# Performance work log

Hardware: AMD Instinct MI355X
Metric: run time of the kernel (lower is better)

Reference implementation:

```python
import jax, jax.numpy as jnp
import numpy as np

N, C_IN, H, W = 256, 256, 28, 28
D = 64        # prototype channel dim (prototype_shape[1])
P = 200       # num prototypes
NCLS = 10


def setup_inputs() -> dict:
    key = jax.random.key(0)
    ks = jax.random.split(key, 6)
    x = jax.random.normal(ks[0], (N, C_IN, H, W), dtype=jnp.float32)
    W1 = jax.random.normal(ks[1], (D, C_IN), dtype=jnp.float32) * 0.05
    b1 = jnp.zeros((D,), dtype=jnp.float32)
    W2 = jax.random.normal(ks[2], (D, D), dtype=jnp.float32) * 0.05
    b2 = jnp.zeros((D,), dtype=jnp.float32)
    prototypes = jax.random.uniform(ks[3], (P, D), dtype=jnp.float32)
    last_W = jax.random.normal(ks[4], (NCLS, P), dtype=jnp.float32) * 0.05
    last_b = jnp.zeros((NCLS,), dtype=jnp.float32)
    return {"x": x, "W1": W1, "b1": b1, "W2": W2, "b2": b2,
            "prototypes": prototypes, "last_W": last_W, "last_b": last_b}


def reference(x, W1, b1, W2, b2, prototypes, last_W, last_b):
    # add_on_layers: 1x1 conv -> relu -> 1x1 conv -> sigmoid (pointwise GEMMs)
    h = jax.nn.relu(jnp.einsum('nchw,oc->nohw', x, W1) + b1[None, :, None, None])
    f = jax.nn.sigmoid(jnp.einsum('nchw,oc->nohw', h, W2) + b2[None, :, None, None])
    # L2 convolution with 1x1 prototypes:
    # conv(x^2, ones) == channel sum of f^2, broadcast over P prototypes
    x2_patch_sum = jnp.sum(f * f, axis=1, keepdims=True)          # (N,1,H,W)
    xp = jnp.einsum('nchw,pc->nphw', f, prototypes)               # (N,P,H,W)
    p2 = jnp.sum(prototypes * prototypes, axis=1)[None, :, None, None]  # (1,P,1,1)
    distances = jax.nn.relu(x2_patch_sum - 2.0 * xp + p2)         # (N,P,H,W)
    # global min-pool over spatial dims (== -maxpool(-d) with full kernel)
    min_distances = jnp.min(distances, axis=(2, 3))               # (N,P)
    # paf == 'linear': similarity = -distance
    prototype_activations = -min_distances
    logits = prototype_activations @ last_W.T + last_b            # (N,NCLS)
    return (logits, min_distances)
```

## Files before the change

kernel.cpp:

```cpp
#include <hip/hip_runtime.h>
#include <hip/hip_bf16.h>

#define NIMG 256
#define CIN  256
#define PIX  784
#define DD   64
#define NP   200
#define NPP  208
#define NCLS 10

#define XS 264
#define HS 72

typedef __attribute__((ext_vector_type(8))) short bf16x8;
typedef __attribute__((ext_vector_type(4))) float f32x4;
typedef __attribute__((ext_vector_type(4))) unsigned int u32x4;

__device__ __forceinline__ unsigned short f2bf(float f) {
    union { float f; unsigned int u; } v; v.f = f;
    unsigned int r = v.u + 0x7fffu + ((v.u >> 16) & 1u);
    return (unsigned short)(r >> 16);
}

__device__ __forceinline__ unsigned int pk2(float a, float b) {
    __hip_bfloat162 p = __float22bfloat162_rn(make_float2(a, b));
    return *(unsigned int*)&p;
}

#define MFMA(a, b, c) __builtin_amdgcn_mfma_f32_16x16x32_bf16((a), (b), (c), 0, 0, 0)

__global__ __launch_bounds__(512, 2)
void proto_fused_kernel(const float* __restrict__ x,
                        const float* __restrict__ W1, const float* __restrict__ b1,
                        const float* __restrict__ W2, const float* __restrict__ b2,
                        const float* __restrict__ proto,
                        const float* __restrict__ lastW, const float* __restrict__ lastb,
                        float* __restrict__ out)
{
    __shared__ __align__(16) unsigned short xlds[64 * XS];
    __shared__ __align__(16) unsigned short w1lds[64 * XS];
    __shared__ __align__(16) unsigned short w2lds[64 * HS];
    __shared__ __align__(16) unsigned short protolds[NPP * HS];
    __shared__ __align__(16) unsigned short htile[64 * HS];
    __shared__ __align__(16) unsigned short ftile[64 * HS];
    __shared__ float p2lds[NPP];
    __shared__ float s2lds[2][64];
    __shared__ float b1lds[DD], b2lds[DD];
    __shared__ unsigned int bmin[NPP];

    const int n    = blockIdx.x;
    const int t    = threadIdx.x;
    const int lane = t & 63;
    const int q    = lane >> 4;
    const int l15  = lane & 15;
    const int wave = t >> 6;
    const int s    = wave & 3;
    const int dh   = wave >> 2;
    const int dt0  = dh * 2, dt1 = dh * 2 + 1;

    for (int i = 0; i < 32; ++i) {
        int idx = t + i * 512;
        w1lds[(idx >> 8) * XS + (idx & 255)] = f2bf(W1[idx]);
    }
    for (int i = 0; i < 8; ++i) {
        int idx = t + i * 512;
        w2lds[(idx >> 6) * HS + (idx & 63)] = f2bf(W2[idx]);
    }
    for (int i = 0; i < 25; ++i) {
        int idx = t + i * 512;
        protolds[(idx >> 6) * HS + (idx & 63)] = f2bf(proto[idx]);
    }
    {
        int p = NP + (t >> 6), d = t & 63;
        protolds[p * HS + d] = 0;
    }
    if (t < DD) { b1lds[t] = b1[t]; b2lds[t] = b2[t]; }
    if (t < NPP) {
        float acc = 0.f;
        if (t < NP) {
            for (int d = 0; d < DD; ++d) { float v = proto[t * DD + d]; acc += v * v; }
        }
        p2lds[t] = acc;
        bmin[t] = 0x7f800000u;
    }

    const int p4  = (t & 15) * 4;
    const int cb8 = (t >> 4) * 8;
    const float* xn = x + (size_t)n * CIN * PIX;

    float4 pf[8];
    auto load_tile = [&](int px0) {
        #pragma unroll
        for (int j = 0; j < 8; ++j) {
            const float* src = xn + (size_t)(cb8 + j) * PIX + px0 + p4;
            float4 v;
            if (px0 + p4 + 3 < PIX) {
                v = *(const float4*)src;
            } else {
                v.x = (px0 + p4 + 0 < PIX) ? src[0] : 0.f;
                v.y = (px0 + p4 + 1 < PIX) ? src[1] : 0.f;
                v.z = (px0 + p4 + 2 < PIX) ? src[2] : 0.f;
                v.w = (px0 + p4 + 3 < PIX) ? src[3] : 0.f;
            }
            pf[j] = v;
        }
    };
    auto store_tile = [&]() {
        #pragma unroll
        for (int r = 0; r < 4; ++r) {
            u32x4 uv;
            uv.x = pk2(((const float*)&pf[0])[r], ((const float*)&pf[1])[r]);
            uv.y = pk2(((const float*)&pf[2])[r], ((const float*)&pf[3])[r]);
            uv.z = pk2(((const float*)&pf[4])[r], ((const float*)&pf[5])[r]);
            uv.w = pk2(((const float*)&pf[6])[r], ((const float*)&pf[7])[r]);
            *(u32x4*)&xlds[(p4 + r) * XS + cb8] = uv;
        }
    };

    load_tile(0);
    store_tile();
    load_tile(64);
    __syncthreads();

    bf16x8 w1f0[8], w1f1[8];
    #pragma unroll
    for (int kk = 0; kk < 8; ++kk) {
        w1f0[kk] = *(const bf16x8*)&w1lds[(dt0 * 16 + l15) * XS + kk * 32 + q * 8];
        w1f1[kk] = *(const bf16x8*)&w1lds[(dt1 * 16 + l15) * XS + kk * 32 + q * 8];
    }
    bf16x8 w2f0[2], w2f1[2];
    #pragma unroll
    for (int kk = 0; kk < 2; ++kk) {
        w2f0[kk] = *(const bf16x8*)&w2lds[(dt0 * 16 + l15) * HS + kk * 32 + q * 8];
        w2f1[kk] = *(const bf16x8*)&w2lds[(dt1 * 16 + l15) * HS + kk * 32 + q * 8];
    }

    for (int tl = 0; tl < 13; ++tl) {
        const int px0 = tl * 64;

        {
            f32x4 acc0 = {0.f, 0.f, 0.f, 0.f}, acc1 = {0.f, 0.f, 0.f, 0.f};
            const int arow = (s * 16 + l15) * XS + q * 8;
            #pragma unroll
            for (int kk = 0; kk < 8; ++kk) {
                bf16x8 a = *(const bf16x8*)&xlds[arow + kk * 32];
                acc0 = MFMA(a, w1f0[kk], acc0);
                acc1 = MFMA(a, w1f1[kk], acc1);
            }
            #pragma unroll
            for (int r = 0; r < 4; ++r) {
                int prow = s * 16 + q * 4 + r;
                float h0 = fmaxf(acc0[r] + b1lds[dt0 * 16 + l15], 0.f);
                float h1 = fmaxf(acc1[r] + b1lds[dt1 * 16 + l15], 0.f);
                htile[prow * HS + dt0 * 16 + l15] = f2bf(h0);
                htile[prow * HS + dt1 * 16 + l15] = f2bf(h1);
            }
        }
        __syncthreads();

        if (tl < 12) store_tile();
        {
            f32x4 acc0 = {0.f, 0.f, 0.f, 0.f}, acc1 = {0.f, 0.f, 0.f, 0.f};
            const int arowH = (s * 16 + l15) * HS + q * 8;
            bf16x8 a0 = *(const bf16x8*)&htile[arowH];
            bf16x8 a1 = *(const bf16x8*)&htile[arowH + 32];
            acc0 = MFMA(a0, w2f0[0], acc0);
            acc0 = MFMA(a1, w2f0[1], acc0);
            acc1 = MFMA(a0, w2f1[0], acc1);
            acc1 = MFMA(a1, w2f1[1], acc1);
            #pragma unroll
            for (int r = 0; r < 4; ++r) {
                int prow = s * 16 + q * 4 + r;
                float z0 = acc0[r] + b2lds[dt0 * 16 + l15];
                float z1 = acc1[r] + b2lds[dt1 * 16 + l15];
                float f0 = __builtin_amdgcn_rcpf(1.0f + __builtin_amdgcn_exp2f(z0 * -1.44269504f));
                float f1 = __builtin_amdgcn_rcpf(1.0f + __builtin_amdgcn_exp2f(z1 * -1.44269504f));
                ftile[prow * HS + dt0 * 16 + l15] = f2bf(f0);
                ftile[prow * HS + dt1 * 16 + l15] = f2bf(f1);
                float v = f0 * f0 + f1 * f1;
                v += __shfl_xor(v, 1, 64);
                v += __shfl_xor(v, 2, 64);
                v += __shfl_xor(v, 4, 64);
                v += __shfl_xor(v, 8, 64);
                if (l15 == 0) s2lds[dh][prow] = v;
            }
        }
        __syncthreads();

        if (tl < 11) load_tile((tl + 2) * 64);
        {
            const int arowF = (s * 16 + l15) * HS + q * 8;
            bf16x8 a0 = *(const bf16x8*)&ftile[arowF];
            bf16x8 a1 = *(const bf16x8*)&ftile[arowF + 32];
            float s2v[4];
            bool  vmask[4];
            #pragma unroll
            for (int r = 0; r < 4; ++r) {
                int pl = s * 16 + q * 4 + r;
                s2v[r]   = s2lds[0][pl] + s2lds[1][pl];
                vmask[r] = (px0 + pl < PIX);
            }
            for (int pt = dh; pt < 13; pt += 2) {
                const int brow = (pt * 16 + l15) * HS + q * 8;
                bf16x8 bb0 = *(const bf16x8*)&protolds[brow];
                bf16x8 bb1 = *(const bf16x8*)&protolds[brow + 32];
                f32x4 acc = {0.f, 0.f, 0.f, 0.f};
                acc = MFMA(a0, bb0, acc);
                acc = MFMA(a1, bb1, acc);
                const int p = pt * 16 + l15;
                const float p2v = p2lds[p];
                float m = 1e30f;
                #pragma unroll
                for (int r = 0; r < 4; ++r) {
                    float dist = fmaxf(s2v[r] - 2.f * acc[r] + p2v, 0.f);
                    if (vmask[r]) m = fminf(m, dist);
                }
                m = fminf(m, __shfl_xor(m, 16, 64));
                m = fminf(m, __shfl_xor(m, 32, 64));
                if (lane < 16) atomicMin(&bmin[p], __float_as_uint(m));
            }
        }
    }
    __syncthreads();

    if (t < NP) {
        out[NIMG * NCLS + (size_t)n * NP + t] = __uint_as_float(bmin[t]);
    }
    if (t < 320) {
        int c = t >> 5, j = t & 31;
        float acc = 0.f;
        for (int p = j; p < NP; p += 32)
            acc += __uint_as_float(bmin[p]) * lastW[c * NP + p];
        acc += __shfl_xor(acc, 1, 32);
        acc += __shfl_xor(acc, 2, 32);
        acc += __shfl_xor(acc, 4, 32);
        acc += __shfl_xor(acc, 8, 32);
        acc += __shfl_xor(acc, 16, 32);
        if (j == 0) out[(size_t)n * NCLS + c] = -acc + lastb[c];
    }
}

extern "C" void kernel_launch(void* const* d_in, const int* in_sizes, int n_in,
                              void* d_out, int out_size, void* d_ws, size_t ws_size,
                              hipStream_t stream) {
    const float* x     = (const float*)d_in[0];
    const float* W1    = (const float*)d_in[1];
    const float* b1    = (const float*)d_in[2];
    const float* W2    = (const float*)d_in[3];
    const float* b2    = (const float*)d_in[4];
    const float* proto = (const float*)d_in[5];
    const float* lastW = (const float*)d_in[6];
    const float* lastb = (const float*)d_in[7];
    float* out = (float*)d_out;

    proto_fused_kernel<<<dim3(NIMG), dim3(512), 0, stream>>>(
        x, W1, b1, W2, b2, proto, lastW, lastb, out);
}
```

Before: 312.3 us.

## Keep prototype fragments and running minima in registers, defer min reduction

```diff
diff --git a/kernel.cpp b/kernel.cpp
--- a/kernel.cpp
+++ b/kernel.cpp
@@ -21,7 +21,6 @@
     unsigned int r = v.u + 0x7fffu + ((v.u >> 16) & 1u);
     return (unsigned short)(r >> 16);
 }
-
 __device__ __forceinline__ unsigned int pk2(float a, float b) {
     __hip_bfloat162 p = __float22bfloat162_rn(make_float2(a, b));
     return *(unsigned int*)&p;
@@ -40,7 +39,6 @@
     __shared__ __align__(16) unsigned short xlds[64 * XS];
     __shared__ __align__(16) unsigned short w1lds[64 * XS];
     __shared__ __align__(16) unsigned short w2lds[64 * HS];
-    __shared__ __align__(16) unsigned short protolds[NPP * HS];
     __shared__ __align__(16) unsigned short htile[64 * HS];
     __shared__ __align__(16) unsigned short ftile[64 * HS];
     __shared__ float p2lds[NPP];
@@ -66,33 +64,48 @@
         int idx = t + i * 512;
         w2lds[(idx >> 6) * HS + (idx & 63)] = f2bf(W2[idx]);
     }
-    for (int i = 0; i < 25; ++i) {
-        int idx = t + i * 512;
-        protolds[(idx >> 6) * HS + (idx & 63)] = f2bf(proto[idx]);
-    }
-    {
-        int p = NP + (t >> 6), d = t & 63;
-        protolds[p * HS + d] = 0;
-    }
     if (t < DD) { b1lds[t] = b1[t]; b2lds[t] = b2[t]; }
     if (t < NPP) {
         float acc = 0.f;
         if (t < NP) {
-            for (int d = 0; d < DD; ++d) { float v = proto[t * DD + d]; acc += v * v; }
+            const float4* pp = (const float4*)(proto + t * DD);
+            #pragma unroll
+            for (int i = 0; i < 16; ++i) {
+                float4 v = pp[i];
+                acc += v.x * v.x + v.y * v.y + v.z * v.z + v.w * v.w;
+            }
         }
         p2lds[t] = acc;
         bmin[t] = 0x7f800000u;
     }
 
-    const int p4  = (t & 15) * 4;
-    const int cb8 = (t >> 4) * 8;
+    bf16x8 pb0[7], pb1[7];
+    #pragma unroll
+    for (int it = 0; it < 7; ++it) {
+        int pt = dh + 2 * it;
+        int p  = pt * 16 + l15;
+        int pr = (p < NP) ? p : (NP - 1);
+        const float4* src = (const float4*)(proto + (size_t)pr * DD + q * 8);
+        float4 a = src[0], b = src[1];
+        float4 c = src[8], d = src[9];
+        union { u32x4 u; bf16x8 h; } cv0, cv1;
+        cv0.u.x = pk2(a.x, a.y); cv0.u.y = pk2(a.z, a.w);
+        cv0.u.z = pk2(b.x, b.y); cv0.u.w = pk2(b.z, b.w);
+        cv1.u.x = pk2(c.x, c.y); cv1.u.y = pk2(c.z, c.w);
+        cv1.u.z = pk2(d.x, d.y); cv1.u.w = pk2(d.z, d.w);
+        pb0[it] = cv0.h; pb1[it] = cv1.h;
+    }
+
+    const int p4   = ((t >> 2) & 15) * 4;
+    const int c8i  = (t & 3) | ((t >> 6) << 2);
+    const int c8   = c8i * 8;
     const float* xn = x + (size_t)n * CIN * PIX;
 
     float4 pf[8];
     auto load_tile = [&](int px0) {
         #pragma unroll
         for (int j = 0; j < 8; ++j) {
-            const float* src = xn + (size_t)(cb8 + j) * PIX + px0 + p4;
+            const float* src = xn + (size_t)(c8 + j) * PIX + px0 + p4;
             float4 v;
             if (px0 + p4 + 3 < PIX) {
                 v = *(const float4*)src;
@@ -113,7 +126,7 @@
             uv.y = pk2(((const float*)&pf[2])[r], ((const float*)&pf[3])[r]);
             uv.z = pk2(((const float*)&pf[4])[r], ((const float*)&pf[5])[r]);
             uv.w = pk2(((const float*)&pf[6])[r], ((const float*)&pf[7])[r]);
-            *(u32x4*)&xlds[(p4 + r) * XS + cb8] = uv;
+            *(u32x4*)&xlds[(p4 + r) * XS + c8] = uv;
         }
     };
 
@@ -134,6 +147,16 @@
         w2f0[kk] = *(const bf16x8*)&w2lds[(dt0 * 16 + l15) * HS + kk * 32 + q * 8];
         w2f1[kk] = *(const bf16x8*)&w2lds[(dt1 * 16 + l15) * HS + kk * 32 + q * 8];
     }
+    float p2r[7];
+    #pragma unroll
+    for (int it = 0; it < 7; ++it) {
+        int pidx = (dh + 2 * it) * 16 + l15;
+        p2r[it] = p2lds[pidx < NPP ? pidx : (NPP - 1)];
+    }
+
+    float rmin[7];
+    #pragma unroll
+    for (int it = 0; it < 7; ++it) rmin[it] = 1e30f;
 
     for (int tl = 0; tl < 13; ++tl) {
         const int px0 = tl * 64;
@@ -159,6 +182,7 @@
         __syncthreads();
 
         if (tl < 12) store_tile();
+        if (tl < 11) load_tile((tl + 2) * 64);
         {
             f32x4 acc0 = {0.f, 0.f, 0.f, 0.f}, acc1 = {0.f, 0.f, 0.f, 0.f};
             const int arowH = (s * 16 + l15) * HS + q * 8;
@@ -182,43 +206,46 @@
                 v += __shfl_xor(v, 2, 64);
                 v += __shfl_xor(v, 4, 64);
                 v += __shfl_xor(v, 8, 64);
-                if (l15 == 0) s2lds[dh][prow] = v;
+                if (l15 == 0)
+                    s2lds[dh][prow] = (px0 + prow < PIX) ? v : 1e30f;
             }
         }
         __syncthreads();
 
-        if (tl < 11) load_tile((tl + 2) * 64);
         {
             const int arowF = (s * 16 + l15) * HS + q * 8;
             bf16x8 a0 = *(const bf16x8*)&ftile[arowF];
             bf16x8 a1 = *(const bf16x8*)&ftile[arowF + 32];
             float s2v[4];
-            bool  vmask[4];
             #pragma unroll
             for (int r = 0; r < 4; ++r) {
                 int pl = s * 16 + q * 4 + r;
-                s2v[r]   = s2lds[0][pl] + s2lds[1][pl];
-                vmask[r] = (px0 + pl < PIX);
-            }
-            for (int pt = dh; pt < 13; pt += 2) {
-                const int brow = (pt * 16 + l15) * HS + q * 8;
-                bf16x8 bb0 = *(const bf16x8*)&protolds[brow];
-                bf16x8 bb1 = *(const bf16x8*)&protolds[brow + 32];
+                s2v[r] = s2lds[0][pl] + s2lds[1][pl];
+            }
+            #pragma unroll
+            for (int it = 0; it < 7; ++it) {
                 f32x4 acc = {0.f, 0.f, 0.f, 0.f};
-                acc = MFMA(a0, bb0, acc);
-                acc = MFMA(a1, bb1, acc);
-                const int p = pt * 16 + l15;
-                const float p2v = p2lds[p];
+                acc = MFMA(a0, pb0[it], acc);
+                acc = MFMA(a1, pb1[it], acc);
                 float m = 1e30f;
                 #pragma unroll
                 for (int r = 0; r < 4; ++r) {
-                    float dist = fmaxf(s2v[r] - 2.f * acc[r] + p2v, 0.f);
-                    if (vmask[r]) m = fminf(m, dist);
+                    float dist = fmaxf(s2v[r] - 2.f * acc[r] + p2r[it], 0.f);
+                    m = fminf(m, dist);
                 }
-                m = fminf(m, __shfl_xor(m, 16, 64));
-                m = fminf(m, __shfl_xor(m, 32, 64));
-                if (lane < 16) atomicMin(&bmin[p], __float_as_uint(m));
-            }
+                rmin[it] = fminf(rmin[it], m);
+            }
+        }
+    }
+
+    #pragma unroll
+    for (int it = 0; it < 7; ++it) {
+        int pt = dh + 2 * it;
+        if (pt < 13) {
+            float m = rmin[it];
+            m = fminf(m, __shfl_xor(m, 16, 64));
+            m = fminf(m, __shfl_xor(m, 32, 64));
+            if (lane < 16) atomicMin(&bmin[pt * 16 + l15], __float_as_uint(m));
         }
     }
     __syncthreads();
```

Measured after the change: 308.9 us. Within noise of the previous version (-1.1%).

## Give each wave independent pixel strips to remove block-wide barriers

Applied to the files above, without the earlier changes.

```diff
diff --git a/kernel.cpp b/kernel.cpp
--- a/kernel.cpp
+++ b/kernel.cpp
@@ -8,6 +8,7 @@
 #define NP   200
 #define NPP  208
 #define NCLS 10
+#define NSTRIP 49
 
 #define XS 264
 #define HS 72
@@ -21,13 +22,13 @@
     unsigned int r = v.u + 0x7fffu + ((v.u >> 16) & 1u);
     return (unsigned short)(r >> 16);
 }
-
 __device__ __forceinline__ unsigned int pk2(float a, float b) {
     __hip_bfloat162 p = __float22bfloat162_rn(make_float2(a, b));
     return *(unsigned int*)&p;
 }
 
 #define MFMA(a, b, c) __builtin_amdgcn_mfma_f32_16x16x32_bf16((a), (b), (c), 0, 0, 0)
+#define LGK() __asm__ volatile("s_waitcnt lgkmcnt(0)" ::: "memory")
 
 __global__ __launch_bounds__(512, 2)
 void proto_fused_kernel(const float* __restrict__ x,
@@ -37,34 +38,72 @@
                         const float* __restrict__ lastW, const float* __restrict__ lastb,
                         float* __restrict__ out)
 {
-    __shared__ __align__(16) unsigned short xlds[64 * XS];
+    __shared__ __align__(16) unsigned short xbuf[8][16 * XS];
     __shared__ __align__(16) unsigned short w1lds[64 * XS];
-    __shared__ __align__(16) unsigned short w2lds[64 * HS];
+    __shared__ __align__(16) unsigned short hbuf[8][16 * HS];
     __shared__ __align__(16) unsigned short protolds[NPP * HS];
-    __shared__ __align__(16) unsigned short htile[64 * HS];
-    __shared__ __align__(16) unsigned short ftile[64 * HS];
     __shared__ float p2lds[NPP];
-    __shared__ float s2lds[2][64];
     __shared__ float b1lds[DD], b2lds[DD];
     __shared__ unsigned int bmin[NPP];
 
     const int n    = blockIdx.x;
     const int t    = threadIdx.x;
     const int lane = t & 63;
+    const int wave = t >> 6;
     const int q    = lane >> 4;
     const int l15  = lane & 15;
-    const int wave = t >> 6;
-    const int s    = wave & 3;
-    const int dh   = wave >> 2;
-    const int dt0  = dh * 2, dt1 = dh * 2 + 1;
+
+    const int sBeg = (wave * NSTRIP) >> 3;
+    const int sEnd = ((wave + 1) * NSTRIP) >> 3;
+
+    const int px4 = ((lane >> 2) & 3) * 4;
+    const int cg  = (lane & 3) | ((lane >> 4) << 2);
+    const int c16 = cg * 16;
+    const float* xn = x + (size_t)n * CIN * PIX;
+
+    float4 pf[16];
+    auto load_strip = [&](int s) {
+        const float* base = xn + s * 16 + px4;
+        #pragma unroll
+        for (int j = 0; j < 16; ++j)
+            pf[j] = *(const float4*)(base + (size_t)(c16 + j) * PIX);
+    };
+    auto store_strip = [&]() {
+        #pragma unroll
+        for (int r = 0; r < 4; ++r) {
+            u32x4 u0, u1;
+            u0.x = pk2(((const float*)&pf[ 0])[r], ((const float*)&pf[ 1])[r]);
+            u0.y = pk2(((const float*)&pf[ 2])[r], ((const float*)&pf[ 3])[r]);
+            u0.z = pk2(((const float*)&pf[ 4])[r], ((const float*)&pf[ 5])[r]);
+            u0.w = pk2(((const float*)&pf[ 6])[r], ((const float*)&pf[ 7])[r]);
+            u1.x = pk2(((const float*)&pf[ 8])[r], ((const float*)&pf[ 9])[r]);
+            u1.y = pk2(((const float*)&pf[10])[r], ((const float*)&pf[11])[r]);
+            u1.z = pk2(((const float*)&pf[12])[r], ((const float*)&pf[13])[r]);
+            u1.w = pk2(((const float*)&pf[14])[r], ((const float*)&pf[15])[r]);
+            *(u32x4*)&xbuf[wave][(px4 + r) * XS + c16]     = u0;
+            *(u32x4*)&xbuf[wave][(px4 + r) * XS + c16 + 8] = u1;
+        }
+    };
+
+    load_strip(sBeg);
+
+    bf16x8 w2f[4][2];
+    #pragma unroll
+    for (int dt = 0; dt < 4; ++dt) {
+        #pragma unroll
+        for (int kk = 0; kk < 2; ++kk) {
+            const float4* src = (const float4*)(W2 + (size_t)(dt * 16 + l15) * DD + kk * 32 + q * 8);
+            float4 a = src[0], b = src[1];
+            union { u32x4 u; bf16x8 h; } cv;
+            cv.u.x = pk2(a.x, a.y); cv.u.y = pk2(a.z, a.w);
+            cv.u.z = pk2(b.x, b.y); cv.u.w = pk2(b.z, b.w);
+            w2f[dt][kk] = cv.h;
+        }
+    }
 
     for (int i = 0; i < 32; ++i) {
         int idx = t + i * 512;
         w1lds[(idx >> 8) * XS + (idx & 255)] = f2bf(W1[idx]);
-    }
-    for (int i = 0; i < 8; ++i) {
-        int idx = t + i * 512;
-        w2lds[(idx >> 6) * HS + (idx & 63)] = f2bf(W2[idx]);
     }
     for (int i = 0; i < 25; ++i) {
         int idx = t + i * 512;
@@ -78,148 +117,118 @@
     if (t < NPP) {
         float acc = 0.f;
         if (t < NP) {
-            for (int d = 0; d < DD; ++d) { float v = proto[t * DD + d]; acc += v * v; }
+            const float4* pp = (const float4*)(proto + t * DD);
+            #pragma unroll
+            for (int i = 0; i < 16; ++i) {
+                float4 v = pp[i];
+                acc += v.x * v.x + v.y * v.y + v.z * v.z + v.w * v.w;
+            }
         }
         p2lds[t] = acc;
         bmin[t] = 0x7f800000u;
     }
-
-    const int p4  = (t & 15) * 4;
-    const int cb8 = (t >> 4) * 8;
-    const float* xn = x + (size_t)n * CIN * PIX;
-
-    float4 pf[8];
-    auto load_tile = [&](int px0) {
-        #pragma unroll
-        for (int j = 0; j < 8; ++j) {
-            const float* src = xn + (size_t)(cb8 + j) * PIX + px0 + p4;
-            float4 v;
-            if (px0 + p4 + 3 < PIX) {
-                v = *(const float4*)src;
-            } else {
-                v.x = (px0 + p4 + 0 < PIX) ? src[0] : 0.f;
-                v.y = (px0 + p4 + 1 < PIX) ? src[1] : 0.f;
-                v.z = (px0 + p4 + 2 < PIX) ? src[2] : 0.f;
-                v.w = (px0 + p4 + 3 < PIX) ? src[3] : 0.f;
+    __syncthreads();
+
+    float b1r[4], b2r[4];
+    #pragma unroll
+    for (int dt = 0; dt < 4; ++dt) {
+        b1r[dt] = b1lds[dt * 16 + l15];
+        b2r[dt] = b2lds[dt * 16 + l15];
+    }
+    float p2r[13];
+    #pragma unroll
+    for (int pt = 0; pt < 13; ++pt) p2r[pt] = p2lds[pt * 16 + l15];
+
+    float rmin[13];
+    #pragma unroll
+    for (int pt = 0; pt < 13; ++pt) rmin[pt] = 1e30f;
+
+    unsigned short* xw = &xbuf[wave][0];
+    unsigned short* hw = &hbuf[wave][0];
+
+    for (int s = sBeg; s < sEnd; ++s) {
+        store_strip();
+        if (s + 1 < sEnd) load_strip(s + 1);
+        LGK();
+
+        f32x4 acc[4] = {{0,0,0,0},{0,0,0,0},{0,0,0,0},{0,0,0,0}};
+        #pragma unroll
+        for (int kk = 0; kk < 8; ++kk) {
+            bf16x8 a = *(const bf16x8*)&xw[l15 * XS + kk * 32 + q * 8];
+            #pragma unroll
+            for (int dt = 0; dt < 4; ++dt) {
+                bf16x8 b = *(const bf16x8*)&w1lds[(dt * 16 + l15) * XS + kk * 32 + q * 8];
+                acc[dt] = MFMA(a, b, acc[dt]);
             }
-            pf[j] = v;
-        }
-    };
-    auto store_tile = [&]() {
+        }
+        #pragma unroll
+        for (int dt = 0; dt < 4; ++dt)
+            #pragma unroll
+            for (int r = 0; r < 4; ++r)
+                hw[(q * 4 + r) * HS + dt * 16 + l15] =
+                    f2bf(fmaxf(acc[dt][r] + b1r[dt], 0.f));
+        LGK();
+
+        bf16x8 ha0 = *(const bf16x8*)&hw[l15 * HS + q * 8];
+        bf16x8 ha1 = *(const bf16x8*)&hw[l15 * HS + 32 + q * 8];
+        f32x4 acc2[4] = {{0,0,0,0},{0,0,0,0},{0,0,0,0},{0,0,0,0}};
+        #pragma unroll
+        for (int dt = 0; dt < 4; ++dt) {
+            acc2[dt] = MFMA(ha0, w2f[dt][0], acc2[dt]);
+            acc2[dt] = MFMA(ha1, w2f[dt][1], acc2[dt]);
+        }
+        float fv[4][4];
+        #pragma unroll
+        for (int dt = 0; dt < 4; ++dt)
+            #pragma unroll
+            for (int r = 0; r < 4; ++r) {
+                float z = acc2[dt][r] + b2r[dt];
+                fv[dt][r] = __builtin_amdgcn_rcpf(1.0f + __builtin_amdgcn_exp2f(z * -1.44269504f));
+            }
+
+        float s2v[4];
         #pragma unroll
         for (int r = 0; r < 4; ++r) {
-            u32x4 uv;
-            uv.x = pk2(((const float*)&pf[0])[r], ((const float*)&pf[1])[r]);
-            uv.y = pk2(((const float*)&pf[2])[r], ((const float*)&pf[3])[r]);
-            uv.z = pk2(((const float*)&pf[4])[r], ((const float*)&pf[5])[r]);
-            uv.w = pk2(((const float*)&pf[6])[r], ((const float*)&pf[7])[r]);
-            *(u32x4*)&xlds[(p4 + r) * XS + cb8] = uv;
-        }
-    };
-
-    load_tile(0);
-    store_tile();
-    load_tile(64);
-    __syncthreads();
-
-    bf16x8 w1f0[8], w1f1[8];
-    #pragma unroll
-    for (int kk = 0; kk < 8; ++kk) {
-        w1f0[kk] = *(const bf16x8*)&w1lds[(dt0 * 16 + l15) * XS + kk * 32 + q * 8];
-        w1f1[kk] = *(const bf16x8*)&w1lds[(dt1 * 16 + l15) * XS + kk * 32 + q * 8];
-    }
-    bf16x8 w2f0[2], w2f1[2];
-    #pragma unroll
-    for (int kk = 0; kk < 2; ++kk) {
-        w2f0[kk] = *(const bf16x8*)&w2lds[(dt0 * 16 + l15) * HS + kk * 32 + q * 8];
-        w2f1[kk] = *(const bf16x8*)&w2lds[(dt1 * 16 + l15) * HS + kk * 32 + q * 8];
-    }
-
-    for (int tl = 0; tl < 13; ++tl) {
-        const int px0 = tl * 64;
-
-        {
-            f32x4 acc0 = {0.f, 0.f, 0.f, 0.f}, acc1 = {0.f, 0.f, 0.f, 0.f};
-            const int arow = (s * 16 + l15) * XS + q * 8;
-            #pragma unroll
-            for (int kk = 0; kk < 8; ++kk) {
-                bf16x8 a = *(const bf16x8*)&xlds[arow + kk * 32];
-                acc0 = MFMA(a, w1f0[kk], acc0);
-                acc1 = MFMA(a, w1f1[kk], acc1);
-            }
-            #pragma unroll
-            for (int r = 0; r < 4; ++r) {
-                int prow = s * 16 + q * 4 + r;
-                float h0 = fmaxf(acc0[r] + b1lds[dt0 * 16 + l15], 0.f);
-                float h1 = fmaxf(acc1[r] + b1lds[dt1 * 16 + l15], 0.f);
-                htile[prow * HS + dt0 * 16 + l15] = f2bf(h0);
-                htile[prow * HS + dt1 * 16 + l15] = f2bf(h1);
-            }
-        }
-        __syncthreads();
-
-        if (tl < 12) store_tile();
-        {
-            f32x4 acc0 = {0.f, 0.f, 0.f, 0.f}, acc1 = {0.f, 0.f, 0.f, 0.f};
-            const int arowH = (s * 16 + l15) * HS + q * 8;
-            bf16x8 a0 = *(const bf16x8*)&htile[arowH];
-            bf16x8 a1 = *(const bf16x8*)&htile[arowH + 32];
-            acc0 = MFMA(a0, w2f0[0], acc0);
-            acc0 = MFMA(a1, w2f0[1], acc0);
-            acc1 = MFMA(a0, w2f1[0], acc1);
-            acc1 = MFMA(a1, w2f1[1], acc1);
-            #pragma unroll
-            for (int r = 0; r < 4; ++r) {
-                int prow = s * 16 + q * 4 + r;
-                float z0 = acc0[r] + b2lds[dt0 * 16 + l15];
-                float z1 = acc1[r] + b2lds[dt1 * 16 + l15];
-                float f0 = __builtin_amdgcn_rcpf(1.0f + __builtin_amdgcn_exp2f(z0 * -1.44269504f));
-                float f1 = __builtin_amdgcn_rcpf(1.0f + __builtin_amdgcn_exp2f(z1 * -1.44269504f));
-                ftile[prow * HS + dt0 * 16 + l15] = f2bf(f0);
-                ftile[prow * HS + dt1 * 16 + l15] = f2bf(f1);
-                float v = f0 * f0 + f1 * f1;
-                v += __shfl_xor(v, 1, 64);
-                v += __shfl_xor(v, 2, 64);
-                v += __shfl_xor(v, 4, 64);
-                v += __shfl_xor(v, 8, 64);
-                if (l15 == 0) s2lds[dh][prow] = v;
-            }
-        }
-        __syncthreads();
-
-        if (tl < 11) load_tile((tl + 2) * 64);
-        {
-            const int arowF = (s * 16 + l15) * HS + q * 8;
-            bf16x8 a0 = *(const bf16x8*)&ftile[arowF];
-            bf16x8 a1 = *(const bf16x8*)&ftile[arowF + 32];
-            float s2v[4];
-            bool  vmask[4];
-            #pragma unroll
-            for (int r = 0; r < 4; ++r) {
-                int pl = s * 16 + q * 4 + r;
-                s2v[r]   = s2lds[0][pl] + s2lds[1][pl];
-                vmask[r] = (px0 + pl < PIX);
-            }
-            for (int pt = dh; pt < 13; pt += 2) {
-                const int brow = (pt * 16 + l15) * HS + q * 8;
-                bf16x8 bb0 = *(const bf16x8*)&protolds[brow];
-                bf16x8 bb1 = *(const bf16x8*)&protolds[brow + 32];
-                f32x4 acc = {0.f, 0.f, 0.f, 0.f};
-                acc = MFMA(a0, bb0, acc);
-                acc = MFMA(a1, bb1, acc);
-                const int p = pt * 16 + l15;
-                const float p2v = p2lds[p];
-                float m = 1e30f;
-                #pragma unroll
-                for (int r = 0; r < 4; ++r) {
-                    float dist = fmaxf(s2v[r] - 2.f * acc[r] + p2v, 0.f);
-                    if (vmask[r]) m = fminf(m, dist);
-                }
-                m = fminf(m, __shfl_xor(m, 16, 64));
-                m = fminf(m, __shfl_xor(m, 32, 64));
-                if (lane < 16) atomicMin(&bmin[p], __float_as_uint(m));
-            }
-        }
+            float v = 0.f;
+            #pragma unroll
+            for (int dt = 0; dt < 4; ++dt) v += fv[dt][r] * fv[dt][r];
+            v += __shfl_xor(v, 1, 64);
+            v += __shfl_xor(v, 2, 64);
+            v += __shfl_xor(v, 4, 64);
+            v += __shfl_xor(v, 8, 64);
+            s2v[r] = v;
+        }
+
+        #pragma unroll
+        for (int dt = 0; dt < 4; ++dt)
+            #pragma unroll
+            for (int r = 0; r < 4; ++r)
+                hw[(q * 4 + r) * HS + dt * 16 + l15] = f2bf(fv[dt][r]);
+        LGK();
+
+        bf16x8 fa0 = *(const bf16x8*)&hw[l15 * HS + q * 8];
+        bf16x8 fa1 = *(const bf16x8*)&hw[l15 * HS + 32 + q * 8];
+        #pragma unroll
+        for (int pt = 0; pt < 13; ++pt) {
+            bf16x8 pb0 = *(const bf16x8*)&protolds[(pt * 16 + l15) * HS + q * 8];
+            bf16x8 pb1 = *(const bf16x8*)&protolds[(pt * 16 + l15) * HS + 32 + q * 8];
+            f32x4 a3 = {0.f, 0.f, 0.f, 0.f};
+            a3 = MFMA(fa0, pb0, a3);
+            a3 = MFMA(fa1, pb1, a3);
+            float m = 1e30f;
+            #pragma unroll
+            for (int r = 0; r < 4; ++r)
+                m = fminf(m, fmaxf(s2v[r] - 2.f * a3[r] + p2r[pt], 0.f));
+            rmin[pt] = fminf(rmin[pt], m);
+        }
+    }
+
+    #pragma unroll
+    for (int pt = 0; pt < 13; ++pt) {
+        float m = rmin[pt];
+        m = fminf(m, __shfl_xor(m, 16, 64));
+        m = fminf(m, __shfl_xor(m, 32, 64));
+        if (lane < 16) atomicMin(&bmin[pt * 16 + l15], __float_as_uint(m));
     }
     __syncthreads();
 
```

Measured after the change: 315.4 us. About the same (+1.0%).
